# Kernel tuning notes

Measured on AMD Instinct MI355X. Metric: run time of the kernel, lower is better.

Reference implementation:

```python
import jax, jax.numpy as jnp
import numpy as np

TEMPERATURE = 8.0  # sqrt(d_head=64)
NEG_INF = -1e15


def setup_inputs() -> dict:
    key = jax.random.key(0)
    k1, k2_, k3, k4, k5, k6 = jax.random.split(key, 6)
    BH, N, D = 16, 2048, 64
    B = 2  # edge batch; BH // B == 8 heads
    return {
        "q": jax.random.normal(k1, (BH, N, D), dtype=jnp.float32),
        "k": jax.random.normal(k2_, (BH, N, D), dtype=jnp.float32),
        "v": jax.random.normal(k3, (BH, N, D), dtype=jnp.float32),
        "k2": jax.random.normal(k4, (BH, N, D), dtype=jnp.float32),
        "mask": jax.random.randint(k5, (BH, 1, N), 0, 2) > 0,
        "edge": jax.random.randint(k6, (B, N, N), 0, 2).astype(jnp.int32),
    }


def reference(q, k, v, k2, mask, edge):
    # attn scores: [bh, n, m]
    attn = jnp.einsum("bnd,bmd->bnm", q, k) / TEMPERATURE
    # torch .repeat along dim0 == tile
    reps = attn.shape[0] // edge.shape[0]
    edge_t = jnp.tile(edge, (reps, 1, 1))
    attn = jnp.where(edge_t == 0, NEG_INF, attn)
    attn = jnp.where(mask, NEG_INF, attn)
    attn = jax.nn.softmax(attn, axis=2)  # dropout p=0 (eval)
    output = jnp.einsum("bnm,bmd->bnd", attn, v)
    # non_linear=False, so no sigmoid
    return (output, attn)
```

## Files before the change

### kernel.cpp

```cpp
#include <hip/hip_runtime.h>
#include <stdint.h>
#include <math.h>

#define BH_ 16
#define N_  2048
#define D_  64
#define NEGV (-1e15f)

typedef __attribute__((ext_vector_type(8))) short bf16x8;
typedef __attribute__((ext_vector_type(8))) unsigned short us8;
typedef __attribute__((ext_vector_type(4))) float f32x4;

#define OFF_MASKU8 0u
#define OFF_MBITS  32768u
#define OFF_EBITS  65536u
#define OFF_QBF    1114112u
#define OFF_KBF    5308416u
#define OFF_VT     9502720u
#define WS_V6      13697024u

#define BARRIER_LGKM() do {                                   \
    asm volatile("s_waitcnt lgkmcnt(0)" ::: "memory");        \
    __builtin_amdgcn_sched_barrier(0);                        \
    __builtin_amdgcn_s_barrier();                             \
    __builtin_amdgcn_sched_barrier(0);                        \
} while (0)

__device__ __forceinline__ unsigned short f2bf(float f) {
    unsigned u = __float_as_uint(f);
    return (unsigned short)((u + 0x7FFFu + ((u >> 16) & 1u)) >> 16);
}

__global__ __launch_bounds__(256)
void prep_all(const float* __restrict__ q, const float* __restrict__ k,
              const float* __restrict__ v, const void* __restrict__ mraw,
              const int* __restrict__ edge,
              unsigned short* __restrict__ qbf, unsigned short* __restrict__ kbf,
              unsigned short* __restrict__ vT,
              unsigned short* __restrict__ e16, unsigned long long* __restrict__ mbits)
{
    __shared__ unsigned short shbuf[64][72];
    __shared__ int flag;
    const int bid = blockIdx.x;
    const int t   = threadIdx.x;

    if (bid < 2048) {
        const int idx = bid * 256 + t;
        const int4* p = (const int4*)(edge + (size_t)idx * 16);
        unsigned m = 0;
        #pragma unroll
        for (int i = 0; i < 4; ++i) {
            const int4 vv = p[i];
            m |= (vv.x != 0 ? 1u : 0u) << (i * 4 + 0);
            m |= (vv.y != 0 ? 1u : 0u) << (i * 4 + 1);
            m |= (vv.z != 0 ? 1u : 0u) << (i * 4 + 2);
            m |= (vv.w != 0 ? 1u : 0u) << (i * 4 + 3);
        }
        e16[idx] = (unsigned short)m;
    } else if (bid < 2560) {
        const int b2 = bid - 2048;
        const int rt = b2 & 31, bh = b2 >> 5;
        const size_t base = ((size_t)bh * N_ + (size_t)rt * 64) * D_;
        #pragma unroll
        for (int i = 0; i < 4; ++i) {
            const int idx = t + i * 256;
            float4 f = *(const float4*)(q + base + (size_t)idx * 4);
            ushort4 s; s.x = f2bf(f.x); s.y = f2bf(f.y); s.z = f2bf(f.z); s.w = f2bf(f.w);
            *(ushort4*)(qbf + base + (size_t)idx * 4) = s;
            f = *(const float4*)(k + base + (size_t)idx * 4);
            s.x = f2bf(f.x); s.y = f2bf(f.y); s.z = f2bf(f.z); s.w = f2bf(f.w);
            *(ushort4*)(kbf + base + (size_t)idx * 4) = s;
            f = *(const float4*)(v + base + (size_t)idx * 4);
            const int row = idx >> 4;
            const int d0  = (idx & 15) * 4;
            shbuf[d0 + 0][row] = f2bf(f.x);
            shbuf[d0 + 1][row] = f2bf(f.y);
            shbuf[d0 + 2][row] = f2bf(f.z);
            shbuf[d0 + 3][row] = f2bf(f.w);
        }
        __syncthreads();
        const int d  = t >> 2;
        const int c4 = (t & 3) * 16;
        const size_t ob = ((size_t)bh * D_ + d) * N_ + (size_t)rt * 64 + c4;
        *(us8*)(vT + ob)     = *(us8*)&shbuf[d][c4];
        *(us8*)(vT + ob + 8) = *(us8*)&shbuf[d][c4 + 8];
    } else {
        const int bh = bid - 2560;
        if (t == 0) flag = 0;
        __syncthreads();
        const int* mi = (const int*)mraw;
        int bad = 0;
        for (int i = t; i < 8192; i += 256)
            if ((unsigned)mi[i] > 1u) bad = 1;
        if (bad) atomicOr(&flag, 1);
        __syncthreads();
        const int is_u8 = flag;
        const uint8_t* m8 = (const uint8_t*)mraw;
        const int w4 = t >> 6, l = t & 63;
        for (int it = 0; it < 8; ++it) {
            const int pos = bh * 2048 + it * 256 + w4 * 64 + l;
            const bool on = is_u8 ? (m8[pos] != 0) : (mi[pos] != 0);
            unsigned long long bal = __ballot(on);
            if (l == 0) mbits[bh * 32 + it * 4 + w4] = bal;
        }
    }
}

__global__ __launch_bounds__(512)
void attn_v9(const unsigned short* __restrict__ qbf,
             const unsigned short* __restrict__ kbf,
             const unsigned short* __restrict__ vT,
             const unsigned long long* __restrict__ ebits,
             const unsigned long long* __restrict__ mbits,
             float* __restrict__ out, float* __restrict__ attn)
{
    __shared__ unsigned short sK[2][4096];
    __shared__ unsigned short sV[2][4096];
    __shared__ char pbuf[8][2048];

    const int bh   = blockIdx.x;
    const int tile = blockIdx.y;
    const int t    = threadIdx.x;
    const int w    = t >> 6;
    const int lane = t & 63;
    const int l15  = lane & 15;
    const int lg   = lane >> 4;
    const int rbase = tile * 128;
    const int myrow = rbase + w * 16 + l15;

    const unsigned short* qb = qbf + (size_t)bh * N_ * D_;
    const unsigned short* kb = kbf + (size_t)bh * N_ * D_;
    const unsigned short* vb = vT  + (size_t)bh * D_ * N_;
    const unsigned long long* ebrow =
        ebits + ((size_t)(bh & 1) * N_ + (size_t)myrow) * 32;
    const unsigned long long* mb = mbits + bh * 32;
    float* outb = out + (size_t)bh * N_ * D_;
    float* arow = attn + (size_t)bh * N_ * N_ + (size_t)myrow * N_ + lg * 4;

    const bf16x8 aq0 = *(const bf16x8*)(qb + (size_t)myrow * D_ + lg * 8);
    const bf16x8 aq1 = *(const bf16x8*)(qb + (size_t)myrow * D_ + lg * 8 + 32);

    const int srow = t >> 3;
    const int t8   = t & 7;
    const int dsw  = srow * 64 + ((t8 ^ (srow & 7)) * 8);

    {
        *(us8*)(sK[0] + dsw) = *(const us8*)(kb + (size_t)t * 8);
        BARRIER_LGKM();
    }
    float lacc = 0.f;
    #pragma unroll 1
    for (int kc = 0; kc < 32; ++kc) {
        const int cur = kc & 1;
        us8 nk0;
        if (kc < 31)
            nk0 = *(const us8*)(kb + (size_t)(kc + 1) * 4096 + (size_t)t * 8);
        const unsigned long long wbits = ebrow[kc] & ~mb[kc];
        const unsigned short* kcur = sK[cur];
        #pragma unroll
        for (int nt = 0; nt < 4; ++nt) {
            const int row = nt * 16 + l15, sw = row & 7;
            const bf16x8 k0 = *(const bf16x8*)(kcur + row * 64 + ((lg ^ sw) * 8));
            const bf16x8 k1 = *(const bf16x8*)(kcur + row * 64 + (((lg + 4) ^ sw) * 8));
            f32x4 c = (f32x4){0.f, 0.f, 0.f, 0.f};
            c = __builtin_amdgcn_mfma_f32_16x16x32_bf16(k0, aq0, c, 0, 0, 0);
            c = __builtin_amdgcn_mfma_f32_16x16x32_bf16(k1, aq1, c, 0, 0, 0);
            const unsigned bits = (unsigned)(wbits >> (nt * 16 + lg * 4)) & 0xFu;
            #pragma unroll
            for (int r = 0; r < 4; ++r)
                lacc += ((bits >> r) & 1u) ? __expf(c[r] * 0.125f) : 0.f;
        }
        if (kc < 31)
            *(us8*)(sK[cur ^ 1] + dsw) = nk0;
        BARRIER_LGKM();
    }
    lacc += __shfl_xor(lacc, 16);
    lacc += __shfl_xor(lacc, 32);
    const float inv = 1.0f / lacc;

    {
        *(us8*)(sK[0] + dsw) = *(const us8*)(kb + (size_t)t * 8);
        *(us8*)(sV[0] + dsw) = *(const us8*)(vb + (size_t)srow * 2048 + t8 * 8);
        BARRIER_LGKM();
    }

    f32x4 o[4];
    #pragma unroll
    for (int nt = 0; nt < 4; ++nt) o[nt] = (f32x4){0.f, 0.f, 0.f, 0.f};

    char* pbw = pbuf[w];
    const int swzP = (l15 & 7) << 4;
    const int ab0 = (l15 * 128 + lg * 16)      ^ swzP;
    const int ab1 = (l15 * 128 + lg * 16 + 64) ^ swzP;

    #pragma unroll 1
    for (int kc = 0; kc < 32; ++kc) {
        const int cur = kc & 1;
        us8 nk0, nv0;
        if (kc < 31) {
            nk0 = *(const us8*)(kb + (size_t)(kc + 1) * 4096 + (size_t)t * 8);
            nv0 = *(const us8*)(vb + (size_t)(kc + 1) * 64 + (size_t)srow * 2048 + t8 * 8);
        }
        const unsigned long long wbits = ebrow[kc] & ~mb[kc];
        const unsigned short* kcur = sK[cur];
        float4 ev[4];
        #pragma unroll
        for (int nt = 0; nt < 4; ++nt) {
            const int row = nt * 16 + l15, sw = row & 7;
            const bf16x8 k0 = *(const bf16x8*)(kcur + row * 64 + ((lg ^ sw) * 8));
            const bf16x8 k1 = *(const bf16x8*)(kcur + row * 64 + (((lg + 4) ^ sw) * 8));
            f32x4 c = (f32x4){0.f, 0.f, 0.f, 0.f};
            c = __builtin_amdgcn_mfma_f32_16x16x32_bf16(k0, aq0, c, 0, 0, 0);
            c = __builtin_amdgcn_mfma_f32_16x16x32_bf16(k1, aq1, c, 0, 0, 0);
            const unsigned bits = (unsigned)(wbits >> (nt * 16 + lg * 4)) & 0xFu;
            float4 e;
            e.x = (bits & 1u) ? __expf(c[0] * 0.125f) * inv : 0.f;
            e.y = (bits & 2u) ? __expf(c[1] * 0.125f) * inv : 0.f;
            e.z = (bits & 4u) ? __expf(c[2] * 0.125f) * inv : 0.f;
            e.w = (bits & 8u) ? __expf(c[3] * 0.125f) * inv : 0.f;
            ev[nt] = e;
            ushort4 pe;
            pe.x = f2bf(e.x); pe.y = f2bf(e.y); pe.z = f2bf(e.z); pe.w = f2bf(e.w);
            const int wbyte = (l15 * 128 + nt * 32 + lg * 8) ^ swzP;
            *(ushort4*)(pbw + wbyte) = pe;
        }
        const bf16x8 ap0 = *(const bf16x8*)(pbw + ab0);
        const bf16x8 ap1 = *(const bf16x8*)(pbw + ab1);
        const unsigned short* vcur = sV[cur];
        #pragma unroll
        for (int nt = 0; nt < 4; ++nt) {
            const int row = nt * 16 + l15, sw = row & 7;
            const bf16x8 bv0 = *(const bf16x8*)(vcur + row * 64 + ((lg ^ sw) * 8));
            const bf16x8 bv1 = *(const bf16x8*)(vcur + row * 64 + (((lg + 4) ^ sw) * 8));
            o[nt] = __builtin_amdgcn_mfma_f32_16x16x32_bf16(ap0, bv0, o[nt], 0, 0, 0);
            o[nt] = __builtin_amdgcn_mfma_f32_16x16x32_bf16(ap1, bv1, o[nt], 0, 0, 0);
        }
        {
            float* astore = arow + kc * 64;
            #pragma unroll
            for (int nt = 0; nt < 4; ++nt)
                *(float4*)(astore + nt * 16) = ev[nt];
        }
        if (kc < 31) {
            *(us8*)(sK[cur ^ 1] + dsw) = nk0;
            *(us8*)(sV[cur ^ 1] + dsw) = nv0;
        }
        BARRIER_LGKM();
    }

    #pragma unroll
    for (int nt = 0; nt < 4; ++nt)
        #pragma unroll
        for (int r = 0; r < 4; ++r)
            outb[(size_t)(rbase + w * 16 + lg * 4 + r) * D_ + nt * 16 + l15] = o[nt][r];
}

__global__ __launch_bounds__(256)
void normalize_mask(const void* __restrict__ mask_raw, uint8_t* __restrict__ mask_out)
{
    __shared__ int is_u8;
    const int t = threadIdx.x;
    if (t == 0) is_u8 = 0;
    __syncthreads();
    const int* mi = (const int*)mask_raw;
    int bad = 0;
    for (int i = t; i < 8192; i += 256)
        if ((unsigned)mi[i] > 1u) bad = 1;
    if (bad) atomicOr(&is_u8, 1);
    __syncthreads();
    const int total = BH_ * N_;
    if (is_u8) {
        const uint8_t* m8 = (const uint8_t*)mask_raw;
        for (int i = t; i < total; i += 256) mask_out[i] = m8[i] ? 1 : 0;
    } else {
        for (int i = t; i < total; i += 256) mask_out[i] = (uint8_t)mi[i];
    }
}

__global__ __launch_bounds__(256)
void attn_fused(const float* __restrict__ q, const float* __restrict__ k,
                const float* __restrict__ v, const uint8_t* __restrict__ mask,
                const int* __restrict__ edge, float* __restrict__ out,
                float* __restrict__ attn)
{
    __shared__ float qsT[D_][64 + 4];
    __shared__ float kt [D_][64 + 4];
    __shared__ float vs [64][D_ + 4];
    const int tile = blockIdx.x, bh = blockIdx.y, t = threadIdx.x;
    const int rg = t >> 4, cg = t & 15, r0 = rg * 4, c0 = cg * 4;
    const int row_base = tile * 64;
    const float* qb = q + (size_t)bh * N_ * D_;
    const float* kb = k + (size_t)bh * N_ * D_;
    const float* vb = v + (size_t)bh * N_ * D_;
    const uint8_t* mbp = mask + (size_t)bh * N_;
    const int* ebp = edge + (size_t)(bh & 1) * N_ * N_;
    float* outb = out + (size_t)bh * N_ * D_;
    float* attnb = attn + (size_t)bh * N_ * N_;
    {
        const int rr = t >> 2, dblk = (t & 3) * 16;
        const float* src = qb + (size_t)(row_base + rr) * D_ + dblk;
        #pragma unroll
        for (int qq = 0; qq < 4; ++qq) {
            float4 val = *(const float4*)(src + qq * 4);
            qsT[dblk + qq*4 + 0][rr] = val.x; qsT[dblk + qq*4 + 1][rr] = val.y;
            qsT[dblk + qq*4 + 2][rr] = val.z; qsT[dblk + qq*4 + 3][rr] = val.w;
        }
    }
    float m_i[4], l_i[4];
    #pragma unroll
    for (int i = 0; i < 4; ++i) { m_i[i] = -INFINITY; l_i[i] = 0.f; }
    for (int kc = 0; kc < 32; ++kc) {
        __syncthreads();
        {
            const int ccr = t >> 2, dblk = (t & 3) * 16;
            const float* src = kb + (size_t)(kc * 64 + ccr) * D_ + dblk;
            #pragma unroll
            for (int qq = 0; qq < 4; ++qq) {
                float4 val = *(const float4*)(src + qq * 4);
                kt[dblk + qq*4 + 0][ccr] = val.x; kt[dblk + qq*4 + 1][ccr] = val.y;
                kt[dblk + qq*4 + 2][ccr] = val.z; kt[dblk + qq*4 + 3][ccr] = val.w;
            }
        }
        __syncthreads();
        float sc[4][4];
        #pragma unroll
        for (int i = 0; i < 4; ++i) { sc[i][0]=sc[i][1]=sc[i][2]=sc[i][3]=0.f; }
        for (int d = 0; d < D_; ++d) {
            const float4 qv = *(const float4*)&qsT[d][r0];
            const float4 kv = *(const float4*)&kt[d][c0];
            #pragma unroll
            for (int i = 0; i < 4; ++i) {
                const float qi = (i==0)?qv.x:(i==1)?qv.y:(i==2)?qv.z:qv.w;
                sc[i][0] = fmaf(qi, kv.x, sc[i][0]); sc[i][1] = fmaf(qi, kv.y, sc[i][1]);
                sc[i][2] = fmaf(qi, kv.z, sc[i][2]); sc[i][3] = fmaf(qi, kv.w, sc[i][3]);
            }
        }
        const int cbase = kc * 64 + c0;
        const uint8_t m0 = mbp[cbase], m1 = mbp[cbase+1], m2 = mbp[cbase+2], m3 = mbp[cbase+3];
        #pragma unroll
        for (int i = 0; i < 4; ++i) {
            const int rglob = row_base + r0 + i;
            const int4 e4 = *(const int4*)(ebp + (size_t)rglob * N_ + cbase);
            float s0 = sc[i][0]*0.125f, s1 = sc[i][1]*0.125f, s2 = sc[i][2]*0.125f, s3 = sc[i][3]*0.125f;
            if (e4.x == 0 || m0) s0 = NEGV; if (e4.y == 0 || m1) s1 = NEGV;
            if (e4.z == 0 || m2) s2 = NEGV; if (e4.w == 0 || m3) s3 = NEGV;
            float cmax = fmaxf(fmaxf(s0,s1), fmaxf(s2,s3));
            cmax = fmaxf(cmax, __shfl_xor(cmax,1)); cmax = fmaxf(cmax, __shfl_xor(cmax,2));
            cmax = fmaxf(cmax, __shfl_xor(cmax,4)); cmax = fmaxf(cmax, __shfl_xor(cmax,8));
            const float nm = fmaxf(m_i[i], cmax);
            float ss = __expf(s0-nm)+__expf(s1-nm)+__expf(s2-nm)+__expf(s3-nm);
            ss += __shfl_xor(ss,1); ss += __shfl_xor(ss,2); ss += __shfl_xor(ss,4); ss += __shfl_xor(ss,8);
            l_i[i] = l_i[i]*__expf(m_i[i]-nm) + ss; m_i[i] = nm;
        }
    }
    float inv_l[4];
    #pragma unroll
    for (int i = 0; i < 4; ++i) inv_l[i] = 1.0f / l_i[i];
    float oacc[4][4];
    #pragma unroll
    for (int i = 0; i < 4; ++i) { oacc[i][0]=oacc[i][1]=oacc[i][2]=oacc[i][3]=0.f; }
    for (int kc = 0; kc < 32; ++kc) {
        __syncthreads();
        {
            const int ccr = t >> 2, dblk = (t & 3) * 16;
            const float* src = kb + (size_t)(kc * 64 + ccr) * D_ + dblk;
            #pragma unroll
            for (int qq = 0; qq < 4; ++qq) {
                float4 val = *(const float4*)(src + qq * 4);
                kt[dblk + qq*4 + 0][ccr] = val.x; kt[dblk + qq*4 + 1][ccr] = val.y;
                kt[dblk + qq*4 + 2][ccr] = val.z; kt[dblk + qq*4 + 3][ccr] = val.w;
            }
            const float* srcv = vb + (size_t)(kc * 64 + ccr) * D_ + dblk;
            #pragma unroll
            for (int qq = 0; qq < 4; ++qq)
                *(float4*)&vs[ccr][dblk + qq * 4] = *(const float4*)(srcv + qq * 4);
        }
        __syncthreads();
        float sc[4][4];
        #pragma unroll
        for (int i = 0; i < 4; ++i) { sc[i][0]=sc[i][1]=sc[i][2]=sc[i][3]=0.f; }
        for (int d = 0; d < D_; ++d) {
            const float4 qv = *(const float4*)&qsT[d][r0];
            const float4 kv = *(const float4*)&kt[d][c0];
            #pragma unroll
            for (int i = 0; i < 4; ++i) {
                const float qi = (i==0)?qv.x:(i==1)?qv.y:(i==2)?qv.z:qv.w;
                sc[i][0] = fmaf(qi, kv.x, sc[i][0]); sc[i][1] = fmaf(qi, kv.y, sc[i][1]);
                sc[i][2] = fmaf(qi, kv.z, sc[i][2]); sc[i][3] = fmaf(qi, kv.w, sc[i][3]);
            }
        }
        const int cbase = kc * 64 + c0;
        const uint8_t m0 = mbp[cbase], m1 = mbp[cbase+1], m2 = mbp[cbase+2], m3 = mbp[cbase+3];
        float p[4][4];
        #pragma unroll
        for (int i = 0; i < 4; ++i) {
            const int rglob = row_base + r0 + i;
            const int4 e4 = *(const int4*)(ebp + (size_t)rglob * N_ + cbase);
            float s0 = sc[i][0]*0.125f, s1 = sc[i][1]*0.125f, s2 = sc[i][2]*0.125f, s3 = sc[i][3]*0.125f;
            if (e4.x == 0 || m0) s0 = NEGV; if (e4.y == 0 || m1) s1 = NEGV;
            if (e4.z == 0 || m2) s2 = NEGV; if (e4.w == 0 || m3) s3 = NEGV;
            p[i][0] = __expf(s0-m_i[i])*inv_l[i]; p[i][1] = __expf(s1-m_i[i])*inv_l[i];
            p[i][2] = __expf(s2-m_i[i])*inv_l[i]; p[i][3] = __expf(s3-m_i[i])*inv_l[i];
            *(float4*)&attnb[(size_t)rglob * N_ + cbase] = make_float4(p[i][0],p[i][1],p[i][2],p[i][3]);
        }
        __syncthreads();
        #pragma unroll
        for (int i = 0; i < 4; ++i)
            *(float4*)&kt[r0 + i][c0] = make_float4(p[i][0],p[i][1],p[i][2],p[i][3]);
        __syncthreads();
        for (int c4 = 0; c4 < 64; c4 += 4) {
            float prr[4][4];
            #pragma unroll
            for (int i = 0; i < 4; ++i) {
                const float4 tmp = *(const float4*)&kt[r0 + i][c4];
                prr[i][0]=tmp.x; prr[i][1]=tmp.y; prr[i][2]=tmp.z; prr[i][3]=tmp.w;
            }
            #pragma unroll
            for (int cc = 0; cc < 4; ++cc) {
                const float4 vv = *(const float4*)&vs[c4 + cc][c0];
                #pragma unroll
                for (int i = 0; i < 4; ++i) {
                    oacc[i][0] = fmaf(prr[i][cc], vv.x, oacc[i][0]);
                    oacc[i][1] = fmaf(prr[i][cc], vv.y, oacc[i][1]);
                    oacc[i][2] = fmaf(prr[i][cc], vv.z, oacc[i][2]);
                    oacc[i][3] = fmaf(prr[i][cc], vv.w, oacc[i][3]);
                }
            }
        }
    }
    #pragma unroll
    for (int i = 0; i < 4; ++i)
        *(float4*)&outb[(size_t)(row_base + r0 + i) * D_ + c0] =
            make_float4(oacc[i][0], oacc[i][1], oacc[i][2], oacc[i][3]);
}

extern "C" void kernel_launch(void* const* d_in, const int* in_sizes, int n_in,
                              void* d_out, int out_size, void* d_ws, size_t ws_size,
                              hipStream_t stream) {
    const float* q    = (const float*)d_in[0];
    const float* k    = (const float*)d_in[1];
    const float* v    = (const float*)d_in[2];
    const void*  mraw = d_in[4];
    const int*   edge = (const int*)d_in[5];

    float* out  = (float*)d_out;
    float* attn = (float*)d_out + (size_t)BH_ * N_ * D_;

    char* ws = (char*)d_ws;

    if (ws_size < (size_t)WS_V6) {
        uint8_t* mask_u8 = (uint8_t*)(ws + OFF_MASKU8);
        normalize_mask<<<1, 256, 0, stream>>>(mraw, mask_u8);
        attn_fused<<<dim3(32, 16), 256, 0, stream>>>(q, k, v, mask_u8, edge, out, attn);
        return;
    }

    unsigned long long* mbits = (unsigned long long*)(ws + OFF_MBITS);
    unsigned short*     e16   = (unsigned short*)(ws + OFF_EBITS);
    unsigned short*     qbf   = (unsigned short*)(ws + OFF_QBF);
    unsigned short*     kbf   = (unsigned short*)(ws + OFF_KBF);
    unsigned short*     vT    = (unsigned short*)(ws + OFF_VT);

    prep_all<<<dim3(2576), 256, 0, stream>>>(q, k, v, mraw, edge,
                                             qbf, kbf, vT, e16, mbits);
    attn_v9<<<dim3(BH_, N_ / 128), 512, 0, stream>>>(
        qbf, kbf, vT, (const unsigned long long*)e16, mbits, out, attn);
}
```

Before: 134.3 us.

## Shrink row tile to 64 with 4 waves and stage two key chunks per barrier

Blocks now have 256 threads (4 waves) and cover 64 query rows, so the grid doubles to 512 blocks. Each pipeline step loads two 64-key chunks of K and V into shared memory, which halves the number of block barriers per pass. The intent is better occupancy and load balance across CUs and less synchronisation overhead. In exchange, each K/V tile is read from global memory by twice as many blocks, and register and LDS use per block go up.

```diff
diff --git a/kernel.cpp b/kernel.cpp
--- a/kernel.cpp
+++ b/kernel.cpp
@@ -106,17 +106,17 @@
     }
 }
 
-__global__ __launch_bounds__(512)
-void attn_v9(const unsigned short* __restrict__ qbf,
-             const unsigned short* __restrict__ kbf,
-             const unsigned short* __restrict__ vT,
-             const unsigned long long* __restrict__ ebits,
-             const unsigned long long* __restrict__ mbits,
-             float* __restrict__ out, float* __restrict__ attn)
+__global__ __launch_bounds__(256)
+void attn_v12(const unsigned short* __restrict__ qbf,
+              const unsigned short* __restrict__ kbf,
+              const unsigned short* __restrict__ vT,
+              const unsigned long long* __restrict__ ebits,
+              const unsigned long long* __restrict__ mbits,
+              float* __restrict__ out, float* __restrict__ attn)
 {
-    __shared__ unsigned short sK[2][4096];
-    __shared__ unsigned short sV[2][4096];
-    __shared__ char pbuf[8][2048];
+    __shared__ unsigned short sK2[2][8192];
+    __shared__ unsigned short sV2[2][8192];
+    __shared__ char pbuf[4][2048];
 
     const int bh   = blockIdx.x;
     const int tile = blockIdx.y;
@@ -125,7 +125,7 @@
     const int lane = t & 63;
     const int l15  = lane & 15;
     const int lg   = lane >> 4;
-    const int rbase = tile * 128;
+    const int rbase = tile * 64;
     const int myrow = rbase + w * 16 + l15;
 
     const unsigned short* qb = qbf + (size_t)bh * N_ * D_;
@@ -140,38 +140,57 @@
     const bf16x8 aq0 = *(const bf16x8*)(qb + (size_t)myrow * D_ + lg * 8);
     const bf16x8 aq1 = *(const bf16x8*)(qb + (size_t)myrow * D_ + lg * 8 + 32);
 
-    const int srow = t >> 3;
-    const int t8   = t & 7;
-    const int dsw  = srow * 64 + ((t8 ^ (srow & 7)) * 8);
+    const int s0row = t >> 3;
+    const int s1row = s0row + 32;
+    const int t8    = t & 7;
+    const int ds0 = s0row * 64 + ((t8 ^ (s0row & 7)) * 8);
+    const int ds1 = s1row * 64 + ((t8 ^ (s1row & 7)) * 8);
 
     {
-        *(us8*)(sK[0] + dsw) = *(const us8*)(kb + (size_t)t * 8);
+        *(us8*)(sK2[0] + ds0)        = *(const us8*)(kb + (size_t)t * 8);
+        *(us8*)(sK2[0] + ds1)        = *(const us8*)(kb + (size_t)(t + 256) * 8);
+        *(us8*)(sK2[0] + 4096 + ds0) = *(const us8*)(kb + 4096 + (size_t)t * 8);
+        *(us8*)(sK2[0] + 4096 + ds1) = *(const us8*)(kb + 4096 + (size_t)(t + 256) * 8);
         BARRIER_LGKM();
     }
     float lacc = 0.f;
     #pragma unroll 1
-    for (int kc = 0; kc < 32; ++kc) {
-        const int cur = kc & 1;
-        us8 nk0;
-        if (kc < 31)
-            nk0 = *(const us8*)(kb + (size_t)(kc + 1) * 4096 + (size_t)t * 8);
-        const unsigned long long wbits = ebrow[kc] & ~mb[kc];
-        const unsigned short* kcur = sK[cur];
-        #pragma unroll
-        for (int nt = 0; nt < 4; ++nt) {
-            const int row = nt * 16 + l15, sw = row & 7;
-            const bf16x8 k0 = *(const bf16x8*)(kcur + row * 64 + ((lg ^ sw) * 8));
-            const bf16x8 k1 = *(const bf16x8*)(kcur + row * 64 + (((lg + 4) ^ sw) * 8));
-            f32x4 c = (f32x4){0.f, 0.f, 0.f, 0.f};
-            c = __builtin_amdgcn_mfma_f32_16x16x32_bf16(k0, aq0, c, 0, 0, 0);
-            c = __builtin_amdgcn_mfma_f32_16x16x32_bf16(k1, aq1, c, 0, 0, 0);
-            const unsigned bits = (unsigned)(wbits >> (nt * 16 + lg * 4)) & 0xFu;
-            #pragma unroll
-            for (int r = 0; r < 4; ++r)
-                lacc += ((bits >> r) & 1u) ? __expf(c[r] * 0.125f) : 0.f;
-        }
-        if (kc < 31)
-            *(us8*)(sK[cur ^ 1] + dsw) = nk0;
+    for (int iv = 0; iv < 16; ++iv) {
+        const int cur = iv & 1;
+        us8 nk[4];
+        if (iv < 15) {
+            const unsigned short* s = kb + (size_t)(2 * iv + 2) * 4096;
+            nk[0] = *(const us8*)(s + (size_t)t * 8);
+            nk[1] = *(const us8*)(s + (size_t)(t + 256) * 8);
+            nk[2] = *(const us8*)(s + 4096 + (size_t)t * 8);
+            nk[3] = *(const us8*)(s + 4096 + (size_t)(t + 256) * 8);
+        }
+        #pragma unroll
+        for (int sub = 0; sub < 2; ++sub) {
+            const int kc = 2 * iv + sub;
+            const unsigned long long wbits = ebrow[kc] & ~mb[kc];
+            const unsigned short* kcur = sK2[cur] + sub * 4096;
+            #pragma unroll
+            for (int nt = 0; nt < 4; ++nt) {
+                const int row = nt * 16 + l15, sw = row & 7;
+                const bf16x8 k0 = *(const bf16x8*)(kcur + row * 64 + ((lg ^ sw) * 8));
+                const bf16x8 k1 = *(const bf16x8*)(kcur + row * 64 + (((lg + 4) ^ sw) * 8));
+                f32x4 c = (f32x4){0.f, 0.f, 0.f, 0.f};
+                c = __builtin_amdgcn_mfma_f32_16x16x32_bf16(k0, aq0, c, 0, 0, 0);
+                c = __builtin_amdgcn_mfma_f32_16x16x32_bf16(k1, aq1, c, 0, 0, 0);
+                const unsigned bits = (unsigned)(wbits >> (nt * 16 + lg * 4)) & 0xFu;
+                #pragma unroll
+                for (int r = 0; r < 4; ++r)
+                    lacc += ((bits >> r) & 1u) ? __expf(c[r] * 0.125f) : 0.f;
+            }
+        }
+        if (iv < 15) {
+            unsigned short* kn = sK2[cur ^ 1];
+            *(us8*)(kn + ds0)        = nk[0];
+            *(us8*)(kn + ds1)        = nk[1];
+            *(us8*)(kn + 4096 + ds0) = nk[2];
+            *(us8*)(kn + 4096 + ds1) = nk[3];
+        }
         BARRIER_LGKM();
     }
     lacc += __shfl_xor(lacc, 16);
@@ -179,8 +198,14 @@
     const float inv = 1.0f / lacc;
 
     {
-        *(us8*)(sK[0] + dsw) = *(const us8*)(kb + (size_t)t * 8);
-        *(us8*)(sV[0] + dsw) = *(const us8*)(vb + (size_t)srow * 2048 + t8 * 8);
+        *(us8*)(sK2[0] + ds0)        = *(const us8*)(kb + (size_t)t * 8);
+        *(us8*)(sK2[0] + ds1)        = *(const us8*)(kb + (size_t)(t + 256) * 8);
+        *(us8*)(sK2[0] + 4096 + ds0) = *(const us8*)(kb + 4096 + (size_t)t * 8);
+        *(us8*)(sK2[0] + 4096 + ds1) = *(const us8*)(kb + 4096 + (size_t)(t + 256) * 8);
+        *(us8*)(sV2[0] + ds0)        = *(const us8*)(vb + (size_t)s0row * 2048 + t8 * 8);
+        *(us8*)(sV2[0] + ds1)        = *(const us8*)(vb + (size_t)s1row * 2048 + t8 * 8);
+        *(us8*)(sV2[0] + 4096 + ds0) = *(const us8*)(vb + 64 + (size_t)s0row * 2048 + t8 * 8);
+        *(us8*)(sV2[0] + 4096 + ds1) = *(const us8*)(vb + 64 + (size_t)s1row * 2048 + t8 * 8);
         BARRIER_LGKM();
     }
 
@@ -194,56 +219,76 @@
     const int ab1 = (l15 * 128 + lg * 16 + 64) ^ swzP;
 
     #pragma unroll 1
-    for (int kc = 0; kc < 32; ++kc) {
-        const int cur = kc & 1;
-        us8 nk0, nv0;
-        if (kc < 31) {
-            nk0 = *(const us8*)(kb + (size_t)(kc + 1) * 4096 + (size_t)t * 8);
-            nv0 = *(const us8*)(vb + (size_t)(kc + 1) * 64 + (size_t)srow * 2048 + t8 * 8);
-        }
-        const unsigned long long wbits = ebrow[kc] & ~mb[kc];
-        const unsigned short* kcur = sK[cur];
-        float4 ev[4];
-        #pragma unroll
-        for (int nt = 0; nt < 4; ++nt) {
-            const int row = nt * 16 + l15, sw = row & 7;
-            const bf16x8 k0 = *(const bf16x8*)(kcur + row * 64 + ((lg ^ sw) * 8));
-            const bf16x8 k1 = *(const bf16x8*)(kcur + row * 64 + (((lg + 4) ^ sw) * 8));
-            f32x4 c = (f32x4){0.f, 0.f, 0.f, 0.f};
-            c = __builtin_amdgcn_mfma_f32_16x16x32_bf16(k0, aq0, c, 0, 0, 0);
-            c = __builtin_amdgcn_mfma_f32_16x16x32_bf16(k1, aq1, c, 0, 0, 0);
-            const unsigned bits = (unsigned)(wbits >> (nt * 16 + lg * 4)) & 0xFu;
-            float4 e;
-            e.x = (bits & 1u) ? __expf(c[0] * 0.125f) * inv : 0.f;
-            e.y = (bits & 2u) ? __expf(c[1] * 0.125f) * inv : 0.f;
-            e.z = (bits & 4u) ? __expf(c[2] * 0.125f) * inv : 0.f;
-            e.w = (bits & 8u) ? __expf(c[3] * 0.125f) * inv : 0.f;
-            ev[nt] = e;
-            ushort4 pe;
-            pe.x = f2bf(e.x); pe.y = f2bf(e.y); pe.z = f2bf(e.z); pe.w = f2bf(e.w);
-            const int wbyte = (l15 * 128 + nt * 32 + lg * 8) ^ swzP;
-            *(ushort4*)(pbw + wbyte) = pe;
-        }
-        const bf16x8 ap0 = *(const bf16x8*)(pbw + ab0);
-        const bf16x8 ap1 = *(const bf16x8*)(pbw + ab1);
-        const unsigned short* vcur = sV[cur];
-        #pragma unroll
-        for (int nt = 0; nt < 4; ++nt) {
-            const int row = nt * 16 + l15, sw = row & 7;
-            const bf16x8 bv0 = *(const bf16x8*)(vcur + row * 64 + ((lg ^ sw) * 8));
-            const bf16x8 bv1 = *(const bf16x8*)(vcur + row * 64 + (((lg + 4) ^ sw) * 8));
-            o[nt] = __builtin_amdgcn_mfma_f32_16x16x32_bf16(ap0, bv0, o[nt], 0, 0, 0);
-            o[nt] = __builtin_amdgcn_mfma_f32_16x16x32_bf16(ap1, bv1, o[nt], 0, 0, 0);
-        }
-        {
-            float* astore = arow + kc * 64;
-            #pragma unroll
-            for (int nt = 0; nt < 4; ++nt)
-                *(float4*)(astore + nt * 16) = ev[nt];
-        }
-        if (kc < 31) {
-            *(us8*)(sK[cur ^ 1] + dsw) = nk0;
-            *(us8*)(sV[cur ^ 1] + dsw) = nv0;
+    for (int iv = 0; iv < 16; ++iv) {
+        const int cur = iv & 1;
+        us8 nk[4], nv[4];
+        if (iv < 15) {
+            const unsigned short* srck = kb + (size_t)(2 * iv + 2) * 4096;
+            const unsigned short* srcv = vb + (size_t)(2 * iv + 2) * 64;
+            nk[0] = *(const us8*)(srck + (size_t)t * 8);
+            nk[1] = *(const us8*)(srck + (size_t)(t + 256) * 8);
+            nk[2] = *(const us8*)(srck + 4096 + (size_t)t * 8);
+            nk[3] = *(const us8*)(srck + 4096 + (size_t)(t + 256) * 8);
+            nv[0] = *(const us8*)(srcv + (size_t)s0row * 2048 + t8 * 8);
+            nv[1] = *(const us8*)(srcv + (size_t)s1row * 2048 + t8 * 8);
+            nv[2] = *(const us8*)(srcv + 64 + (size_t)s0row * 2048 + t8 * 8);
+            nv[3] = *(const us8*)(srcv + 64 + (size_t)s1row * 2048 + t8 * 8);
+        }
+        #pragma unroll
+        for (int sub = 0; sub < 2; ++sub) {
+            const int kc = 2 * iv + sub;
+            const unsigned long long wbits = ebrow[kc] & ~mb[kc];
+            const unsigned short* kcur = sK2[cur] + sub * 4096;
+            float4 ev[4];
+            #pragma unroll
+            for (int nt = 0; nt < 4; ++nt) {
+                const int row = nt * 16 + l15, sw = row & 7;
+                const bf16x8 k0 = *(const bf16x8*)(kcur + row * 64 + ((lg ^ sw) * 8));
+                const bf16x8 k1 = *(const bf16x8*)(kcur + row * 64 + (((lg + 4) ^ sw) * 8));
+                f32x4 c = (f32x4){0.f, 0.f, 0.f, 0.f};
+                c = __builtin_amdgcn_mfma_f32_16x16x32_bf16(k0, aq0, c, 0, 0, 0);
+                c = __builtin_amdgcn_mfma_f32_16x16x32_bf16(k1, aq1, c, 0, 0, 0);
+                const unsigned bits = (unsigned)(wbits >> (nt * 16 + lg * 4)) & 0xFu;
+                float4 e;
+                e.x = (bits & 1u) ? __expf(c[0] * 0.125f) * inv : 0.f;
+                e.y = (bits & 2u) ? __expf(c[1] * 0.125f) * inv : 0.f;
+                e.z = (bits & 4u) ? __expf(c[2] * 0.125f) * inv : 0.f;
+                e.w = (bits & 8u) ? __expf(c[3] * 0.125f) * inv : 0.f;
+                ev[nt] = e;
+                ushort4 pe;
+                pe.x = f2bf(e.x); pe.y = f2bf(e.y); pe.z = f2bf(e.z); pe.w = f2bf(e.w);
+                const int wbyte = (l15 * 128 + nt * 32 + lg * 8) ^ swzP;
+                *(ushort4*)(pbw + wbyte) = pe;
+            }
+            const bf16x8 ap0 = *(const bf16x8*)(pbw + ab0);
+            const bf16x8 ap1 = *(const bf16x8*)(pbw + ab1);
+            const unsigned short* vcur = sV2[cur] + sub * 4096;
+            #pragma unroll
+            for (int nt = 0; nt < 4; ++nt) {
+                const int row = nt * 16 + l15, sw = row & 7;
+                const bf16x8 bv0 = *(const bf16x8*)(vcur + row * 64 + ((lg ^ sw) * 8));
+                const bf16x8 bv1 = *(const bf16x8*)(vcur + row * 64 + (((lg + 4) ^ sw) * 8));
+                o[nt] = __builtin_amdgcn_mfma_f32_16x16x32_bf16(ap0, bv0, o[nt], 0, 0, 0);
+                o[nt] = __builtin_amdgcn_mfma_f32_16x16x32_bf16(ap1, bv1, o[nt], 0, 0, 0);
+            }
+            {
+                float* astore = arow + kc * 64;
+                #pragma unroll
+                for (int nt = 0; nt < 4; ++nt)
+                    *(float4*)(astore + nt * 16) = ev[nt];
+            }
+        }
+        if (iv < 15) {
+            unsigned short* kn = sK2[cur ^ 1];
+            unsigned short* vn = sV2[cur ^ 1];
+            *(us8*)(kn + ds0)        = nk[0];
+            *(us8*)(kn + ds1)        = nk[1];
+            *(us8*)(kn + 4096 + ds0) = nk[2];
+            *(us8*)(kn + 4096 + ds1) = nk[3];
+            *(us8*)(vn + ds0)        = nv[0];
+            *(us8*)(vn + ds1)        = nv[1];
+            *(us8*)(vn + 4096 + ds0) = nv[2];
+            *(us8*)(vn + 4096 + ds1) = nv[3];
         }
         BARRIER_LGKM();
     }
@@ -463,6 +508,6 @@
 
     prep_all<<<dim3(2576), 256, 0, stream>>>(q, k, v, mraw, edge,
                                              qbf, kbf, vT, e16, mbits);
-    attn_v9<<<dim3(BH_, N_ / 128), 512, 0, stream>>>(
+    attn_v12<<<dim3(BH_, N_ / 64), 256, 0, stream>>>(
         qbf, kbf, vT, (const unsigned long long*)e16, mbits, out, attn);
 }
```

Result: faster. 121.7 us (-9.4%).
